# Optimization experiments

Hardware: AMD Instinct MI355X
Metric: run time of the kernel (lower is better)

Reference implementation:

```python
import jax, jax.numpy as jnp
import numpy as np
import math

SEQ_LEN = 720
PRED_LEN = 720
CHANNELS = 862
BATCH = 64
IN_LEN = SEQ_LEN // 2  # seq_len is even -> no padding branch


def dct2_ortho_matrix(N):
    # Orthonormal DCT-II matrix D so that dct(x, norm='ortho') = x @ D.T along last axis
    n = jnp.arange(N, dtype=jnp.float32)
    k = n[:, None]
    D = jnp.cos(jnp.pi * (n[None, :] + 0.5) * k / N) * jnp.sqrt(2.0 / N)
    D = D.at[0].multiply(1.0 / jnp.sqrt(2.0))
    return D  # [N, N], row k = frequency k


def setup_inputs() -> dict:
    key = jax.random.key(0)
    ks = jax.random.split(key, 7)
    x = jax.random.normal(ks[0], (BATCH, SEQ_LEN, CHANNELS), dtype=jnp.float32)
    # depthwise 1x1 convs == per-channel scale + bias
    w1 = jax.random.normal(ks[1], (CHANNELS,), dtype=jnp.float32) * 0.1
    b1 = jax.random.normal(ks[2], (CHANNELS,), dtype=jnp.float32) * 0.1
    w2 = jax.random.normal(ks[3], (CHANNELS,), dtype=jnp.float32) * 0.1
    b2 = jax.random.normal(ks[4], (CHANNELS,), dtype=jnp.float32) * 0.1
    # Linear(in_len, pred_len): W [pred_len, in_len], b [pred_len]
    W_lo = jax.random.normal(ks[5], (PRED_LEN, IN_LEN), dtype=jnp.float32) / math.sqrt(IN_LEN)
    b_lo = jax.random.normal(ks[6], (PRED_LEN,), dtype=jnp.float32) * 0.01
    return {"x": x, "w1": w1, "b1": b1, "w2": w2, "b2": b2, "W_lo": W_lo, "b_lo": b_lo}


def reference(x, w1, b1, w2, b2, W_lo, b_lo):
    B, L, C = x.shape
    xt = jnp.transpose(x, (0, 2, 1))              # [B, C, L]
    seq_mean = jnp.mean(xt, axis=-1, keepdims=True)
    xt = xt - seq_mean
    # depthwise low-pass conv, kernel [1,1]/sqrt(2), stride 2
    lp = xt.reshape(B, C, L // 2, 2).sum(-1) / jnp.sqrt(jnp.float32(2.0))  # [B, C, N]
    N = L // 2
    D = dct2_ortho_matrix(N)
    xd = jnp.einsum('bcn,kn->bck', lp, D) / N     # DCT-II ortho along last axis, scaled
    # x += conv1x1_1(conv1x1_2(x)) -- depthwise 1x1 convs are per-channel affine
    y = (xd * w2[:, None] + b2[:, None]) * w1[:, None] + b1[:, None]
    xd = xd + y
    out = jnp.einsum('bcn,pn->bcp', xd, W_lo) + b_lo  # Linear(in_len -> pred_len)
    out = out + seq_mean                           # [B, C, pred_len]
    return jnp.transpose(out, (0, 2, 1))           # [B, pred_len, C]
```

## Files before the change

kernel.cpp:

```cpp
#include <hip/hip_runtime.h>
#include <hip/hip_bf16.h>
#include <cstdint>

#define SEQ   720
#define PRED  720
#define CH    862
#define NB    64
#define NIN   360
#define KP    384
#define CP    896
#define PP    768
#define BK    32

typedef __attribute__((ext_vector_type(8))) short s16x8;
typedef __attribute__((ext_vector_type(4))) float f32x4;
typedef __attribute__((ext_vector_type(2))) float f32x2;
typedef unsigned int u32;
typedef unsigned short u16;

__device__ __forceinline__ u16 to_bf16u(float f){
  __hip_bfloat16 h = __float2bfloat16(f);
  return *reinterpret_cast<u16*>(&h);
}

__global__ __launch_bounds__(256) void k_dct(float* __restrict__ Dm){
  int idx = blockIdx.x*256 + threadIdx.x;
  if (idx >= NIN*NIN) return;
  int n = idx / NIN, m = idx % NIN;
  int r = ((2*m+1)*n) % (4*NIN);
  float ang = (float)r * (float)(3.14159265358979323846 / 720.0);
  float v = cosf(ang) * 0.07453559924999299f;
  if (n == 0) v *= 0.7071067811865476f;
  Dm[idx] = v;
}

__global__ __launch_bounds__(384) void k_mmat(const float* __restrict__ Wlo, const float* __restrict__ Dm,
                                              u16* __restrict__ Mbf, float* __restrict__ Srow,
                                              float* __restrict__ Slo){
  int p = blockIdx.x;
  int t = threadIdx.x;
  if (p >= PRED){
    Mbf[(size_t)p*KP + t] = 0;
    if (t == 0){ Srow[p] = 0.f; Slo[p] = 0.f; }
    return;
  }
  __shared__ float Wrow[NIN];
  __shared__ float redM[6], redW[6];
  if (t < NIN) Wrow[t] = Wlo[(size_t)p*NIN + t];
  __syncthreads();
  float acc = 0.f;
  if (t < NIN){
    const float* Dc = Dm + t;
    #pragma unroll 4
    for (int n = 0; n < NIN; n++) acc += Wrow[n] * Dc[(size_t)n*NIN];
    acc *= (1.0f/360.0f);
  }
  Mbf[(size_t)p*KP + t] = (t < NIN) ? to_bf16u(acc) : (u16)0;
  float mv = (t < NIN) ? acc : 0.f;
  float wv = (t < NIN) ? Wrow[t] : 0.f;
  #pragma unroll
  for (int off = 32; off > 0; off >>= 1){
    mv += __shfl_down(mv, off);
    wv += __shfl_down(wv, off);
  }
  int wid = t >> 6, lid = t & 63;
  if (lid == 0){ redM[wid] = mv; redW[wid] = wv; }
  __syncthreads();
  if (t == 0){
    float sm = 0.f, sw = 0.f;
    #pragma unroll
    for (int i = 0; i < 6; i++){ sm += redM[i]; sw += redW[i]; }
    Srow[p] = sm; Slo[p] = sw;
  }
}

__global__ __launch_bounds__(256) void k_pre(const float* __restrict__ x, u16* __restrict__ pairB,
                                             float* __restrict__ meanw){
  int b  = blockIdx.y;
  int c0 = blockIdx.x * 64;
  int t  = threadIdx.x;
  int c16  = t & 15;
  int mrow = t >> 4;
  int w    = t >> 6;
  __shared__ u16  pl[192][66];
  __shared__ float red[4][64];
  const float rs2 = 0.7071067811865476f;
  int cb = c0 + c16*4;
  bool full = (cb + 3 < CH);
  const float* xb = x + (size_t)b*SEQ*CH + cb;
  float s0=0.f, s1=0.f, s2=0.f, s3=0.f;
  int rowc = t >> 2;
  int mq0  = t & 3;
  size_t rbase = ((size_t)b*CP + c0 + rowc) * KP;

  #pragma unroll 1
  for (int h = 0; h < 2; h++){
    #pragma unroll 1
    for (int ml = mrow; ml < 192; ml += 16){
      int m = h*192 + ml;
      float p0=0.f, p1=0.f, p2=0.f, p3=0.f;
      if (m < NIN){
        const float* r0 = xb + (size_t)(2*m)*CH;
        float a0,a1,a2,a3, e0,e1,e2,e3;
        if (full){
          f32x4 va = *reinterpret_cast<const f32x4*>(r0);
          f32x2 vb = *reinterpret_cast<const f32x2*>(r0 + CH);
          f32x2 vc = *reinterpret_cast<const f32x2*>(r0 + CH + 2);
          a0=va.x; a1=va.y; a2=va.z; a3=va.w;
          e0=vb.x; e1=vb.y; e2=vc.x; e3=vc.y;
        } else {
          a0 = (cb+0<CH)? r0[0]:0.f; a1 = (cb+1<CH)? r0[1]:0.f;
          a2 = (cb+2<CH)? r0[2]:0.f; a3 = (cb+3<CH)? r0[3]:0.f;
          e0 = (cb+0<CH)? r0[CH+0]:0.f; e1 = (cb+1<CH)? r0[CH+1]:0.f;
          e2 = (cb+2<CH)? r0[CH+2]:0.f; e3 = (cb+3<CH)? r0[CH+3]:0.f;
        }
        p0=a0+e0; p1=a1+e1; p2=a2+e2; p3=a3+e3;
        s0+=p0; s1+=p1; s2+=p2; s3+=p3;
      }
      u32 lo = (u32)to_bf16u(p0*rs2) | ((u32)to_bf16u(p1*rs2) << 16);
      u32 hi = (u32)to_bf16u(p2*rs2) | ((u32)to_bf16u(p3*rs2) << 16);
      *reinterpret_cast<u32*>(&pl[ml][c16*4 + 0]) = lo;
      *reinterpret_cast<u32*>(&pl[ml][c16*4 + 2]) = hi;
    }
    __syncthreads();
    #pragma unroll
    for (int i = 0; i < 6; i++){
      int mg = mq0 + 4*i;
      u16 vals[8];
      #pragma unroll
      for (int j = 0; j < 8; j++) vals[j] = pl[mg*8 + j][rowc];
      uint4 pk;
      pk.x = (u32)vals[0] | ((u32)vals[1] << 16);
      pk.y = (u32)vals[2] | ((u32)vals[3] << 16);
      pk.z = (u32)vals[4] | ((u32)vals[5] << 16);
      pk.w = (u32)vals[6] | ((u32)vals[7] << 16);
      *reinterpret_cast<uint4*>(pairB + rbase + h*192 + (size_t)mg*8) = pk;
    }
    __syncthreads();
  }

  s0 += __shfl_down(s0, 32); s1 += __shfl_down(s1, 32);
  s2 += __shfl_down(s2, 32); s3 += __shfl_down(s3, 32);
  s0 += __shfl_down(s0, 16); s1 += __shfl_down(s1, 16);
  s2 += __shfl_down(s2, 16); s3 += __shfl_down(s3, 16);
  if ((t & 63) < 16){
    f32x4 rv; rv.x=s0; rv.y=s1; rv.z=s2; rv.w=s3;
    *reinterpret_cast<f32x4*>(&red[w][c16*4]) = rv;
  }
  __syncthreads();
  if (t < 64){
    float mean = (red[0][t] + red[1][t] + red[2][t] + red[3][t]) * (1.0f/SEQ);
    meanw[(size_t)b*CP + c0 + t] = mean;
  }
}

#define GLOAD_LDS16(gp, lp_) __builtin_amdgcn_global_load_lds( \
    (const __attribute__((address_space(1))) u32*)(gp), \
    (__attribute__((address_space(3))) u32*)(lp_), 16, 0, 0)

__global__ __launch_bounds__(256, 4) void k_gemm(const u16* __restrict__ Apack, const u16* __restrict__ Mbf,
                                              const float* __restrict__ Srow, const float* __restrict__ Slo,
                                              const float* __restrict__ meanw,
                                              const float* __restrict__ w1, const float* __restrict__ b1,
                                              const float* __restrict__ w2, const float* __restrict__ b2,
                                              const float* __restrict__ blo,
                                              float* __restrict__ out){
  int bid = blockIdx.x;
  int idx = (bid & 7) * 336 + (bid >> 3);
  int pt  = idx % 6;
  int rem = idx / 6;
  int ct  = rem % 7;
  int b   = rem / 7;

  int t  = threadIdx.x;
  int w  = t >> 6, l = t & 63;
  int wr = w >> 1, wc = w & 1;

  __shared__ __align__(16) char smem[32768];
  u16 (*As)[128*BK] = reinterpret_cast<u16(*)[128*BK]>(smem);
  u16 (*Bs)[128*BK] = reinterpret_cast<u16(*)[128*BK]>(smem + 16384);
  float (*wbuf)[16][132] = reinterpret_cast<float(*)[16][132]>(smem);

  f32x4 acc[4][4] = {};

  const u16* Abase = Apack + ((size_t)b*CP + (size_t)ct*128) * KP;
  const u16* Bbase = Mbf + (size_t)pt*128*KP;
  int srow = t >> 2;
  int squad = t & 3;
  int row16 = l & 15, kb = l >> 4;
  int sperm = (srow >> 1) & 3;
  int rperm = (row16 >> 1) & 3;

#define STAGE(bufi, k0) do { \
    GLOAD_LDS16(Abase + (size_t)(srow)*KP + (k0) + ((squad^sperm))*8,      &As[bufi][(srow)*BK + squad*8]); \
    GLOAD_LDS16(Abase + (size_t)(64 + srow)*KP + (k0) + ((squad^sperm))*8, &As[bufi][(64 + srow)*BK + squad*8]); \
    GLOAD_LDS16(Bbase + (size_t)(srow)*KP + (k0) + ((squad^sperm))*8,      &Bs[bufi][(srow)*BK + squad*8]); \
    GLOAD_LDS16(Bbase + (size_t)(64 + srow)*KP + (k0) + ((squad^sperm))*8, &Bs[bufi][(64 + srow)*BK + squad*8]); \
  } while(0)

  STAGE(0, 0);
  for (int ks = 0; ks < 12; ks++){
    int cur = ks & 1;
    if (ks < 11){
      STAGE(cur ^ 1, (ks + 1) * BK);
      asm volatile("s_waitcnt vmcnt(4)" ::: "memory");
    } else {
      asm volatile("s_waitcnt vmcnt(0)" ::: "memory");
    }
    __builtin_amdgcn_s_barrier();
    s16x8 af[4], bfr[4];
    #pragma unroll
    for (int mi = 0; mi < 4; mi++)
      af[mi] = *reinterpret_cast<const s16x8*>(&As[cur][(wr*64 + mi*16 + row16)*BK + (kb^rperm)*8]);
    #pragma unroll
    for (int ni = 0; ni < 4; ni++)
      bfr[ni] = *reinterpret_cast<const s16x8*>(&Bs[cur][(wc*64 + ni*16 + row16)*BK + (kb^rperm)*8]);
    __builtin_amdgcn_s_setprio(1);
    #pragma unroll
    for (int mi = 0; mi < 4; mi++)
      #pragma unroll
      for (int ni = 0; ni < 4; ni++)
        acc[mi][ni] = __builtin_amdgcn_mfma_f32_16x16x32_bf16(af[mi], bfr[ni], acc[mi][ni], 0, 0, 0);
    __builtin_amdgcn_s_setprio(0);
    __builtin_amdgcn_s_barrier();
  }
  __syncthreads();

  int c32 = t & 31;
  int cb4 = ct*128 + c32*4;
  float sc4[4], of4[4], cn4[4], bc4[4];
  #pragma unroll
  for (int j = 0; j < 4; j++){
    int c = cb4 + j;
    bool v = (c < CH);
    float w1v = v ? w1[c] : 0.f, w2v = v ? w2[c] : 0.f;
    float b1v = v ? b1[c] : 0.f, b2v = v ? b2[c] : 0.f;
    float mv  = v ? meanw[(size_t)b*CP + c] : 0.f;
    sc4[j] = 1.f + w1v*w2v;
    of4[j] = w1v*b2v + b1v;
    cn4[j] = mv;
    bc4[j] = 1.4142135623730951f * sc4[j] * mv;
  }
  bool cfull = (cb4 + 3 < CH);
  size_t outb = (size_t)b*PRED*CH;
  int prow = t >> 5;

  #pragma unroll
  for (int ni = 0; ni < 4; ni++){
    #pragma unroll
    for (int mi = 0; mi < 4; mi++)
      #pragma unroll
      for (int r = 0; r < 4; r++)
        wbuf[wc][row16][wr*64 + mi*16 + kb*4 + r] = acc[mi][ni][r];
    __syncthreads();
    #pragma unroll
    for (int k = 0; k < 4; k++){
      int wcp   = k >> 1;
      int p_loc = (k & 1)*8 + prow;
      int p = pt*128 + wcp*64 + ni*16 + p_loc;
      if (p < PRED){
        f32x4 g = *reinterpret_cast<const f32x4*>(&wbuf[wcp][p_loc][c32*4]);
        float sp = Srow[p], sl = Slo[p], bl = blo[p];
        f32x4 ov;
        #pragma unroll
        for (int j = 0; j < 4; j++)
          ov[j] = sc4[j]*g[j] + (cn4[j] - bc4[j]*sp + of4[j]*sl + bl);
        float* op = &out[outb + (size_t)p*CH + cb4];
        if (cfull){
          *reinterpret_cast<f32x4*>(op) = ov;
        } else {
          #pragma unroll
          for (int j = 0; j < 4; j++)
            if (cb4 + j < CH) op[j] = ov[j];
        }
      }
    }
    __syncthreads();
  }
}

extern "C" void kernel_launch(void* const* d_in, const int* in_sizes, int n_in,
                              void* d_out, int out_size, void* d_ws, size_t ws_size,
                              hipStream_t stream)
{
  const float* x   = (const float*)d_in[0];
  const float* w1  = (const float*)d_in[1];
  const float* b1  = (const float*)d_in[2];
  const float* w2  = (const float*)d_in[3];
  const float* b2  = (const float*)d_in[4];
  const float* Wlo = (const float*)d_in[5];
  const float* blo = (const float*)d_in[6];
  float* out = (float*)d_out;

  char* ws = (char*)d_ws;
  float* Dm    = (float*)(ws);
  u16*   Mbf   = (u16*)(ws + 518400);
  float* Srow  = (float*)(ws + 518400 + 589824);
  float* Slo   = (float*)(ws + 518400 + 589824 + 3072);
  u16*   pairB = (u16*)(ws + 518400 + 589824 + 6144);
  float* meanw = (float*)(ws + 518400 + 589824 + 6144 + 44040192);

  k_dct<<<dim3((NIN*NIN + 255)/256), dim3(256), 0, stream>>>(Dm);
  k_mmat<<<dim3(PP), dim3(384), 0, stream>>>(Wlo, Dm, Mbf, Srow, Slo);
  k_pre<<<dim3(CP/64, NB), dim3(256), 0, stream>>>(x, pairB, meanw);
  k_gemm<<<dim3(6*7*NB), dim3(256), 0, stream>>>(pairB, Mbf, Srow, Slo, meanw,
                                                 w1, b1, w2, b2, blo, out);
}
```

Before: 154.6 us.

## Compute folded weight matrix with bf16 MFMA GEMM instead of scalar loop

Replaces the scalar per-row computation of M = W_lo·D/360 with a prep kernel that builds the transposed DCT and W_lo in padded bf16, followed by a small MFMA tiled GEMM that writes bf16 M. Srow is now computed in closed form from the first column of W_lo, because the row sums of the DCT matrix vanish except for the DC term. The main GEMM's A fragments are loaded per row-tile inside the loop to lower register pressure. The GEMM runs with only 18 blocks, and rounding W_lo and D to bf16 adds error to M.

```diff
diff --git a/kernel.cpp b/kernel.cpp
--- a/kernel.cpp
+++ b/kernel.cpp
@@ -23,54 +23,132 @@
   return *reinterpret_cast<u16*>(&h);
 }
 
-__global__ __launch_bounds__(256) void k_dct(float* __restrict__ Dm){
-  int idx = blockIdx.x*256 + threadIdx.x;
-  if (idx >= NIN*NIN) return;
-  int n = idx / NIN, m = idx % NIN;
-  int r = ((2*m+1)*n) % (4*NIN);
-  float ang = (float)r * (float)(3.14159265358979323846 / 720.0);
-  float v = cosf(ang) * 0.07453559924999299f;
-  if (n == 0) v *= 0.7071067811865476f;
-  Dm[idx] = v;
-}
-
-__global__ __launch_bounds__(384) void k_mmat(const float* __restrict__ Wlo, const float* __restrict__ Dm,
-                                              u16* __restrict__ Mbf, float* __restrict__ Srow,
-                                              float* __restrict__ Slo){
-  int p = blockIdx.x;
-  int t = threadIdx.x;
-  if (p >= PRED){
-    Mbf[(size_t)p*KP + t] = 0;
-    if (t == 0){ Srow[p] = 0.f; Slo[p] = 0.f; }
-    return;
-  }
-  __shared__ float Wrow[NIN];
-  __shared__ float redM[6], redW[6];
-  if (t < NIN) Wrow[t] = Wlo[(size_t)p*NIN + t];
+__global__ __launch_bounds__(256) void k_prep0(const float* __restrict__ Wlo,
+                                               u16* __restrict__ Dt, u16* __restrict__ Wbf,
+                                               float* __restrict__ Srow, float* __restrict__ Slo){
+  int bid = blockIdx.x, t = threadIdx.x;
+  if (bid < 576){
+    int idx = bid*256 + t;
+    int m = idx / 384, n = idx % 384;
+    u16 v = 0;
+    if (m < NIN && n < NIN){
+      int r = ((2*m+1)*n) % (4*NIN);
+      float ang = (float)r * (float)(3.14159265358979323846 / 720.0);
+      float x = cosf(ang) * 0.07453559924999299f;
+      if (n == 0) x *= 0.7071067811865476f;
+      v = to_bf16u(x);
+    }
+    Dt[idx] = v;
+  } else if (bid < 1728){
+    int idx = (bid - 576)*256 + t;
+    int p = idx / 384, n = idx % 384;
+    u16 v = 0;
+    if (p < PRED && n < NIN) v = to_bf16u(Wlo[(size_t)p*NIN + n]);
+    Wbf[idx] = v;
+  } else {
+    int w = t >> 6, l = t & 63;
+    int p = (bid - 1728)*4 + w;
+    if (p < PRED){
+      const float* row = Wlo + (size_t)p*NIN;
+      float s = 0.f;
+      for (int i = l; i < NIN; i += 64) s += row[i];
+      #pragma unroll
+      for (int off = 32; off > 0; off >>= 1) s += __shfl_down(s, off);
+      if (l == 0){
+        Slo[p]  = s;
+        Srow[p] = row[0] * 0.05270462766947299f;
+      }
+    }
+  }
+}
+
+#define GLOAD_LDS16(gp, lp_) __builtin_amdgcn_global_load_lds( \
+    (const __attribute__((address_space(1))) u32*)(gp), \
+    (__attribute__((address_space(3))) u32*)(lp_), 16, 0, 0)
+
+__global__ __launch_bounds__(256, 4) void k_mgemm(const u16* __restrict__ Wbf, const u16* __restrict__ Dt,
+                                                  u16* __restrict__ Mbf){
+  int bid = blockIdx.x;
+  int pt = bid % 6;
+  int mt = bid / 6;
+
+  int t  = threadIdx.x;
+  int w  = t >> 6, l = t & 63;
+  int wr = w >> 1, wc = w & 1;
+
+  __shared__ __align__(16) char smem[32768];
+  u16 (*As)[128*BK] = reinterpret_cast<u16(*)[128*BK]>(smem);
+  u16 (*Bs)[128*BK] = reinterpret_cast<u16(*)[128*BK]>(smem + 16384);
+  float (*wb2)[132] = reinterpret_cast<float(*)[132]>(smem);
+
+  f32x4 acc[4][4] = {};
+
+  const u16* Abase = Wbf + (size_t)pt*128*KP;
+  const u16* Bbase = Dt + (size_t)mt*128*KP;
+  int srow = t >> 2;
+  int squad = t & 3;
+  int row16 = l & 15, kb = l >> 4;
+  int sperm = (srow >> 1) & 3;
+  int rperm = (row16 >> 1) & 3;
+
+#define STAGEM(bufi, k0) do { \
+    GLOAD_LDS16(Abase + (size_t)(srow)*KP + (k0) + ((squad^sperm))*8,      &As[bufi][(srow)*BK + squad*8]); \
+    GLOAD_LDS16(Abase + (size_t)(64 + srow)*KP + (k0) + ((squad^sperm))*8, &As[bufi][(64 + srow)*BK + squad*8]); \
+    GLOAD_LDS16(Bbase + (size_t)(srow)*KP + (k0) + ((squad^sperm))*8,      &Bs[bufi][(srow)*BK + squad*8]); \
+    GLOAD_LDS16(Bbase + (size_t)(64 + srow)*KP + (k0) + ((squad^sperm))*8, &Bs[bufi][(64 + srow)*BK + squad*8]); \
+  } while(0)
+
+  STAGEM(0, 0);
+  for (int ks = 0; ks < 12; ks++){
+    int cur = ks & 1;
+    if (ks < 11){
+      STAGEM(cur ^ 1, (ks + 1) * BK);
+      asm volatile("s_waitcnt vmcnt(4)" ::: "memory");
+    } else {
+      asm volatile("s_waitcnt vmcnt(0)" ::: "memory");
+    }
+    __builtin_amdgcn_s_barrier();
+    const u16* aB = &As[cur][(wr*64 + row16)*BK + (kb^rperm)*8];
+    const u16* bB = &Bs[cur][(wc*64 + row16)*BK + (kb^rperm)*8];
+    s16x8 bfr[4];
+    #pragma unroll
+    for (int ni = 0; ni < 4; ni++)
+      bfr[ni] = *reinterpret_cast<const s16x8*>(bB + ni*16*BK);
+    #pragma unroll
+    for (int mi = 0; mi < 4; mi++){
+      s16x8 af = *reinterpret_cast<const s16x8*>(aB + mi*16*BK);
+      #pragma unroll
+      for (int ni = 0; ni < 4; ni++)
+        acc[mi][ni] = __builtin_amdgcn_mfma_f32_16x16x32_bf16(af, bfr[ni], acc[mi][ni], 0, 0, 0);
+    }
+    __builtin_amdgcn_s_barrier();
+  }
   __syncthreads();
-  float acc = 0.f;
-  if (t < NIN){
-    const float* Dc = Dm + t;
-    #pragma unroll 4
-    for (int n = 0; n < NIN; n++) acc += Wrow[n] * Dc[(size_t)n*NIN];
-    acc *= (1.0f/360.0f);
-  }
-  Mbf[(size_t)p*KP + t] = (t < NIN) ? to_bf16u(acc) : (u16)0;
-  float mv = (t < NIN) ? acc : 0.f;
-  float wv = (t < NIN) ? Wrow[t] : 0.f;
-  #pragma unroll
-  for (int off = 32; off > 0; off >>= 1){
-    mv += __shfl_down(mv, off);
-    wv += __shfl_down(wv, off);
-  }
-  int wid = t >> 6, lid = t & 63;
-  if (lid == 0){ redM[wid] = mv; redW[wid] = wv; }
-  __syncthreads();
-  if (t == 0){
-    float sm = 0.f, sw = 0.f;
-    #pragma unroll
-    for (int i = 0; i < 6; i++){ sm += redM[i]; sw += redW[i]; }
-    Srow[p] = sm; Slo[p] = sw;
+
+  const float inv360 = 1.0f/360.0f;
+  #pragma unroll 1
+  for (int mi = 0; mi < 4; mi++){
+    #pragma unroll
+    for (int ni = 0; ni < 4; ni++)
+      #pragma unroll
+      for (int r = 0; r < 4; r++)
+        wb2[wr*16 + kb*4 + r][wc*64 + ni*16 + row16] = acc[mi][ni][r];
+    __syncthreads();
+    #pragma unroll
+    for (int it = 0; it < 2; it++){
+      int wi = it*256 + t;
+      int rl = wi >> 4, seg = wi & 15;
+      int p = pt*128 + (rl>>4)*64 + mi*16 + (rl & 15);
+      f32x4 g0 = *reinterpret_cast<const f32x4*>(&wb2[rl][seg*8]);
+      f32x4 g1 = *reinterpret_cast<const f32x4*>(&wb2[rl][seg*8 + 4]);
+      uint4 pk;
+      pk.x = (u32)to_bf16u(g0.x*inv360) | ((u32)to_bf16u(g0.y*inv360) << 16);
+      pk.y = (u32)to_bf16u(g0.z*inv360) | ((u32)to_bf16u(g0.w*inv360) << 16);
+      pk.z = (u32)to_bf16u(g1.x*inv360) | ((u32)to_bf16u(g1.y*inv360) << 16);
+      pk.w = (u32)to_bf16u(g1.z*inv360) | ((u32)to_bf16u(g1.w*inv360) << 16);
+      *reinterpret_cast<uint4*>(&Mbf[(size_t)p*KP + mt*128 + seg*8]) = pk;
+    }
+    __syncthreads();
   }
 }
 
@@ -154,10 +232,6 @@
   }
 }
 
-#define GLOAD_LDS16(gp, lp_) __builtin_amdgcn_global_load_lds( \
-    (const __attribute__((address_space(1))) u32*)(gp), \
-    (__attribute__((address_space(3))) u32*)(lp_), 16, 0, 0)
-
 __global__ __launch_bounds__(256, 4) void k_gemm(const u16* __restrict__ Apack, const u16* __restrict__ Mbf,
                                               const float* __restrict__ Srow, const float* __restrict__ Slo,
                                               const float* __restrict__ meanw,
@@ -208,19 +282,20 @@
       asm volatile("s_waitcnt vmcnt(0)" ::: "memory");
     }
     __builtin_amdgcn_s_barrier();
-    s16x8 af[4], bfr[4];
-    #pragma unroll
-    for (int mi = 0; mi < 4; mi++)
-      af[mi] = *reinterpret_cast<const s16x8*>(&As[cur][(wr*64 + mi*16 + row16)*BK + (kb^rperm)*8]);
+    const u16* aB = &As[cur][(wr*64 + row16)*BK + (kb^rperm)*8];
+    const u16* bB = &Bs[cur][(wc*64 + row16)*BK + (kb^rperm)*8];
+    s16x8 bfr[4];
     #pragma unroll
     for (int ni = 0; ni < 4; ni++)
-      bfr[ni] = *reinterpret_cast<const s16x8*>(&Bs[cur][(wc*64 + ni*16 + row16)*BK + (kb^rperm)*8]);
+      bfr[ni] = *reinterpret_cast<const s16x8*>(bB + ni*16*BK);
     __builtin_amdgcn_s_setprio(1);
     #pragma unroll
-    for (int mi = 0; mi < 4; mi++)
+    for (int mi = 0; mi < 4; mi++){
+      s16x8 af = *reinterpret_cast<const s16x8*>(aB + mi*16*BK);
       #pragma unroll
       for (int ni = 0; ni < 4; ni++)
-        acc[mi][ni] = __builtin_amdgcn_mfma_f32_16x16x32_bf16(af[mi], bfr[ni], acc[mi][ni], 0, 0, 0);
+        acc[mi][ni] = __builtin_amdgcn_mfma_f32_16x16x32_bf16(af, bfr[ni], acc[mi][ni], 0, 0, 0);
+    }
     __builtin_amdgcn_s_setprio(0);
     __builtin_amdgcn_s_barrier();
   }
@@ -293,15 +368,16 @@
   float* out = (float*)d_out;
 
   char* ws = (char*)d_ws;
-  float* Dm    = (float*)(ws);
-  u16*   Mbf   = (u16*)(ws + 518400);
-  float* Srow  = (float*)(ws + 518400 + 589824);
-  float* Slo   = (float*)(ws + 518400 + 589824 + 3072);
-  u16*   pairB = (u16*)(ws + 518400 + 589824 + 6144);
-  float* meanw = (float*)(ws + 518400 + 589824 + 6144 + 44040192);
-
-  k_dct<<<dim3((NIN*NIN + 255)/256), dim3(256), 0, stream>>>(Dm);
-  k_mmat<<<dim3(PP), dim3(384), 0, stream>>>(Wlo, Dm, Mbf, Srow, Slo);
+  u16*   Dt    = (u16*)(ws);
+  u16*   Wbf   = (u16*)(ws + 294912);
+  u16*   Mbf   = (u16*)(ws + 884736);
+  float* Srow  = (float*)(ws + 1474560);
+  float* Slo   = (float*)(ws + 1477632);
+  u16*   pairB = (u16*)(ws + 1480704);
+  float* meanw = (float*)(ws + 45520896);
+
+  k_prep0<<<dim3(1908), dim3(256), 0, stream>>>(Wlo, Dt, Wbf, Srow, Slo);
+  k_mgemm<<<dim3(18), dim3(256), 0, stream>>>(Wbf, Dt, Mbf);
   k_pre<<<dim3(CP/64, NB), dim3(256), 0, stream>>>(x, pairB, meanw);
   k_gemm<<<dim3(6*7*NB), dim3(256), 0, stream>>>(pairB, Mbf, Srow, Slo, meanw,
                                                  w1, b1, w2, b2, blo, out);
```

New measurement: 154.7 us. Within noise of the previous version (+0.1%).

## Shrink GEMM tile to 64x64 single-wave blocks and drop barriers

Applied to the files above, without the earlier changes.

Restructures the bf16 MFMA GEMM from 256-thread blocks computing 128x128 output tiles to 64-thread single-wave blocks computing 64x64 tiles. The grid grows fourfold with a matching block-index swizzle. Because each block is a single wave, all workgroup barriers and syncthreads are replaced by explicit s_waitcnt instructions, and the epilogue staging buffer shrinks to one wave's slice. The aim is to remove barrier stalls and raise occupancy. The cost is less reuse of each loaded tile, so global and L2 traffic for A and B roughly doubles.

```diff
diff --git a/kernel.cpp b/kernel.cpp
--- a/kernel.cpp
+++ b/kernel.cpp
@@ -158,44 +158,42 @@
     (const __attribute__((address_space(1))) u32*)(gp), \
     (__attribute__((address_space(3))) u32*)(lp_), 16, 0, 0)
 
-__global__ __launch_bounds__(256, 4) void k_gemm(const u16* __restrict__ Apack, const u16* __restrict__ Mbf,
-                                              const float* __restrict__ Srow, const float* __restrict__ Slo,
-                                              const float* __restrict__ meanw,
-                                              const float* __restrict__ w1, const float* __restrict__ b1,
-                                              const float* __restrict__ w2, const float* __restrict__ b2,
-                                              const float* __restrict__ blo,
-                                              float* __restrict__ out){
+__global__ __launch_bounds__(64) void k_gemm(const u16* __restrict__ Apack, const u16* __restrict__ Mbf,
+                                             const float* __restrict__ Srow, const float* __restrict__ Slo,
+                                             const float* __restrict__ meanw,
+                                             const float* __restrict__ w1, const float* __restrict__ b1,
+                                             const float* __restrict__ w2, const float* __restrict__ b2,
+                                             const float* __restrict__ blo,
+                                             float* __restrict__ out){
   int bid = blockIdx.x;
-  int idx = (bid & 7) * 336 + (bid >> 3);
-  int pt  = idx % 6;
-  int rem = idx / 6;
-  int ct  = rem % 7;
-  int b   = rem / 7;
-
-  int t  = threadIdx.x;
-  int w  = t >> 6, l = t & 63;
-  int wr = w >> 1, wc = w & 1;
-
-  __shared__ __align__(16) char smem[32768];
-  u16 (*As)[128*BK] = reinterpret_cast<u16(*)[128*BK]>(smem);
-  u16 (*Bs)[128*BK] = reinterpret_cast<u16(*)[128*BK]>(smem + 16384);
-  float (*wbuf)[16][132] = reinterpret_cast<float(*)[16][132]>(smem);
+  int idx = (bid & 7) * 1344 + (bid >> 3);
+  int pt  = idx % 12;
+  int rem = idx / 12;
+  int ct  = rem % 14;
+  int b   = rem / 14;
+
+  int l = threadIdx.x;
+
+  __shared__ __align__(16) u16 AsB[2][64*32];
+  __shared__ __align__(16) u16 BsB[2][64*32];
+  float (*wbuf)[68] = reinterpret_cast<float(*)[68]>(&AsB[0][0]);
 
   f32x4 acc[4][4] = {};
 
-  const u16* Abase = Apack + ((size_t)b*CP + (size_t)ct*128) * KP;
-  const u16* Bbase = Mbf + (size_t)pt*128*KP;
-  int srow = t >> 2;
-  int squad = t & 3;
+  const u16* Abase = Apack + ((size_t)b*CP + (size_t)ct*64) * KP;
+  const u16* Bbase = Mbf + (size_t)pt*64*KP;
   int row16 = l & 15, kb = l >> 4;
-  int sperm = (srow >> 1) & 3;
   int rperm = (row16 >> 1) & 3;
 
 #define STAGE(bufi, k0) do { \
-    GLOAD_LDS16(Abase + (size_t)(srow)*KP + (k0) + ((squad^sperm))*8,      &As[bufi][(srow)*BK + squad*8]); \
-    GLOAD_LDS16(Abase + (size_t)(64 + srow)*KP + (k0) + ((squad^sperm))*8, &As[bufi][(64 + srow)*BK + squad*8]); \
-    GLOAD_LDS16(Bbase + (size_t)(srow)*KP + (k0) + ((squad^sperm))*8,      &Bs[bufi][(srow)*BK + squad*8]); \
-    GLOAD_LDS16(Bbase + (size_t)(64 + srow)*KP + (k0) + ((squad^sperm))*8, &Bs[bufi][(64 + srow)*BK + squad*8]); \
+    _Pragma("unroll") \
+    for (int j_ = 0; j_ < 4; j_++){ \
+      int r_ = j_*16 + (l >> 2); \
+      int q_ = l & 3; \
+      int sp_ = (r_ >> 1) & 3; \
+      GLOAD_LDS16(Abase + (size_t)r_*KP + (k0) + ((q_^sp_))*8, &AsB[bufi][r_*32 + q_*8]); \
+      GLOAD_LDS16(Bbase + (size_t)r_*KP + (k0) + ((q_^sp_))*8, &BsB[bufi][r_*32 + q_*8]); \
+    } \
   } while(0)
 
   STAGE(0, 0);
@@ -203,18 +201,17 @@
     int cur = ks & 1;
     if (ks < 11){
       STAGE(cur ^ 1, (ks + 1) * BK);
-      asm volatile("s_waitcnt vmcnt(4)" ::: "memory");
+      asm volatile("s_waitcnt vmcnt(8)" ::: "memory");
     } else {
       asm volatile("s_waitcnt vmcnt(0)" ::: "memory");
     }
-    __builtin_amdgcn_s_barrier();
     s16x8 af[4], bfr[4];
     #pragma unroll
     for (int mi = 0; mi < 4; mi++)
-      af[mi] = *reinterpret_cast<const s16x8*>(&As[cur][(wr*64 + mi*16 + row16)*BK + (kb^rperm)*8]);
+      af[mi] = *reinterpret_cast<const s16x8*>(&AsB[cur][(mi*16 + row16)*32 + (kb^rperm)*8]);
     #pragma unroll
     for (int ni = 0; ni < 4; ni++)
-      bfr[ni] = *reinterpret_cast<const s16x8*>(&Bs[cur][(wc*64 + ni*16 + row16)*BK + (kb^rperm)*8]);
+      bfr[ni] = *reinterpret_cast<const s16x8*>(&BsB[cur][(ni*16 + row16)*32 + (kb^rperm)*8]);
     __builtin_amdgcn_s_setprio(1);
     #pragma unroll
     for (int mi = 0; mi < 4; mi++)
@@ -222,12 +219,11 @@
       for (int ni = 0; ni < 4; ni++)
         acc[mi][ni] = __builtin_amdgcn_mfma_f32_16x16x32_bf16(af[mi], bfr[ni], acc[mi][ni], 0, 0, 0);
     __builtin_amdgcn_s_setprio(0);
-    __builtin_amdgcn_s_barrier();
-  }
-  __syncthreads();
-
-  int c32 = t & 31;
-  int cb4 = ct*128 + c32*4;
+  }
+  asm volatile("s_waitcnt lgkmcnt(0) vmcnt(0)" ::: "memory");
+
+  int cq = l & 15, pg = l >> 4;
+  int cb4 = ct*64 + cq*4;
   float sc4[4], of4[4], cn4[4], bc4[4];
   #pragma unroll
   for (int j = 0; j < 4; j++){
@@ -235,7 +231,7 @@
     bool v = (c < CH);
     float w1v = v ? w1[c] : 0.f, w2v = v ? w2[c] : 0.f;
     float b1v = v ? b1[c] : 0.f, b2v = v ? b2[c] : 0.f;
-    float mv  = v ? meanw[(size_t)b*CP + c] : 0.f;
+    float mv  = meanw[(size_t)b*CP + c];
     sc4[j] = 1.f + w1v*w2v;
     of4[j] = w1v*b2v + b1v;
     cn4[j] = mv;
@@ -243,7 +239,6 @@
   }
   bool cfull = (cb4 + 3 < CH);
   size_t outb = (size_t)b*PRED*CH;
-  int prow = t >> 5;
 
   #pragma unroll
   for (int ni = 0; ni < 4; ni++){
@@ -251,15 +246,13 @@
     for (int mi = 0; mi < 4; mi++)
       #pragma unroll
       for (int r = 0; r < 4; r++)
-        wbuf[wc][row16][wr*64 + mi*16 + kb*4 + r] = acc[mi][ni][r];
-    __syncthreads();
-    #pragma unroll
-    for (int k = 0; k < 4; k++){
-      int wcp   = k >> 1;
-      int p_loc = (k & 1)*8 + prow;
-      int p = pt*128 + wcp*64 + ni*16 + p_loc;
+        wbuf[row16][mi*16 + kb*4 + r] = acc[mi][ni][r];
+    #pragma unroll
+    for (int q = 0; q < 4; q++){
+      int pi = q*4 + pg;
+      int p = pt*64 + ni*16 + pi;
       if (p < PRED){
-        f32x4 g = *reinterpret_cast<const f32x4*>(&wbuf[wcp][p_loc][c32*4]);
+        f32x4 g = *reinterpret_cast<const f32x4*>(&wbuf[pi][cq*4]);
         float sp = Srow[p], sl = Slo[p], bl = blo[p];
         f32x4 ov;
         #pragma unroll
@@ -275,7 +268,7 @@
         }
       }
     }
-    __syncthreads();
+    asm volatile("s_waitcnt lgkmcnt(0)" ::: "memory");
   }
 }
 
@@ -303,6 +296,6 @@
   k_dct<<<dim3((NIN*NIN + 255)/256), dim3(256), 0, stream>>>(Dm);
   k_mmat<<<dim3(PP), dim3(384), 0, stream>>>(Wlo, Dm, Mbf, Srow, Slo);
   k_pre<<<dim3(CP/64, NB), dim3(256), 0, stream>>>(x, pairB, meanw);
-  k_gemm<<<dim3(6*7*NB), dim3(256), 0, stream>>>(pairB, Mbf, Srow, Slo, meanw,
-                                                 w1, b1, w2, b2, blo, out);
-}
+  k_gemm<<<dim3(NB*14*12), dim3(64), 0, stream>>>(pairB, Mbf, Srow, Slo, meanw,
+                                                  w1, b1, w2, b2, blo, out);
+}
```

After: 182.7 us. 1.18x slower.
